# Optimization experiments

Hardware: AMD Instinct MI355X
Metric: run time of the kernel (lower is better)

Reference implementation:

```python
import jax, jax.numpy as jnp
import numpy as np

RATE = 0.1
RANDOM_PORTION = 0.1


def setup_inputs() -> dict:
    key = jax.random.key(0)
    x = jax.random.normal(key, (32, 524288), dtype=jnp.float32)
    return {"x": x}


def reference(x) -> jnp.ndarray:
    # Training-mode forward of RandomTopKModifier.
    b = x.shape[0]
    xf = x.reshape(b, -1)                      # [B, N]
    n = xf.shape[1]
    k = max(1, round(RATE * n))

    # 1) top-k by magnitude (indices only; unsorted is fine, set-equivalent)
    _, topk_idx = jax.lax.top_k(jnp.abs(xf), k)            # [B, k] int32

    # 2) build per-element sampling probabilities:
    #    random_portion mass spread over the N-k non-topk slots,
    #    (1 - random_portion) mass spread over the k topk slots.
    rows = jnp.arange(b)[:, None]                           # [B, 1]
    probs = jnp.full_like(xf, RANDOM_PORTION / (n - k))
    probs = probs.at[rows, topk_idx].set((1.0 - RANDOM_PORTION) / k)

    # 3) weighted sampling of k indices WITHOUT replacement
    #    (torch.multinomial(probs, k)) via the Gumbel-top-k trick.
    g = jax.random.gumbel(jax.random.key(42), xf.shape, dtype=xf.dtype)
    _, sel_idx = jax.lax.top_k(jnp.log(probs) + g, k)       # [B, k]

    # 4) scatter a binary mask and apply it
    mask = jnp.zeros_like(xf).at[rows, sel_idx].set(1.0)
    return (mask * xf).reshape(x.shape)
```

## Files before the change

kernel.cpp:

```cpp
#include <hip/hip_runtime.h>
#include <stdint.h>


static constexpr uint32_t BB = 32;
static constexpr uint32_t NN = 524288;
static constexpr uint32_t KK = 52429;
static constexpr uint32_t W = 64;
static constexpr uint32_t CHUNK = NN / W;
static constexpr uint32_t SEGCAP1 = 1024;
static constexpr uint32_t CAP1 = W * SEGCAP1;
static constexpr uint32_t SEGCAP2 = 1280;
static constexpr uint32_t CAP2 = W * SEGCAP2;
static constexpr uint32_t SELCAP = 512;
static constexpr uint32_t SENT = 0xFFFFFFFFu;
static constexpr uint32_t T1KEY = 0x3FD00000u;
static constexpr uint32_t LO1 = T1KEY;
static constexpr uint32_t LO2 = 0x3EC4CCCCu;

__device__ __forceinline__ float xla_logf(float xin) {
#pragma clang fp contract(off)
  float x = fmaxf(xin, __uint_as_float(0x00800000u));
  uint32_t bits = __float_as_uint(x);
  float e = (float)((int)(bits >> 23) - 126);
  x = __uint_as_float((bits & 0x807fffffu) | 0x3f000000u);
  bool mlt = x < 0.707106781186547524f;
  float tmp = mlt ? x : 0.0f;
  x = x - 1.0f;
  e = e - (mlt ? 1.0f : 0.0f);
  x = x + tmp;
  float x2 = x * x;
  float x3 = x2 * x;
  float y, y1, y2;
  y  = 7.0376836292E-2f * x + -1.1514610310E-1f;
  y1 = -1.2420140846E-1f * x + 1.4249322787E-1f;
  y2 = 2.0000714765E-1f * x + -2.4999993993E-1f;
  y  = y * x + 1.1676998740E-1f;
  y1 = y1 * x + -1.6668057665E-1f;
  y2 = y2 * x + 3.3333331174E-1f;
  y  = y * x3 + y1;
  y  = y * x3 + y2;
  y  = y * x3;
  y1 = e * -2.12194440e-4f;
  tmp = x2 * 0.5f;
  y = y + y1;
  x = x - tmp;
  y2 = e * 0.693359375f;
  x = x + y;
  x = x + y2;
  return x;
}

__device__ __forceinline__ float c_top_val()  { return xla_logf((float)((1.0 - 0.1) / 52429.0)); }
__device__ __forceinline__ float c_rand_val() { return xla_logf((float)(0.1 / 471859.0)); }

__device__ __forceinline__ uint32_t tf_bits(uint32_t i) {
  const uint32_t ks0 = 0u, ks1 = 42u, ks2 = 0x1BD11BDAu ^ 42u;
  uint32_t x0 = 0u + ks0;
  uint32_t x1 = i + ks1;
#define TFR(r) { x0 += x1; x1 = (x1 << (r)) | (x1 >> (32 - (r))); x1 ^= x0; }
  TFR(13) TFR(15) TFR(26) TFR(6)
  x0 += ks1; x1 += ks2 + 1u;
  TFR(17) TFR(29) TFR(16) TFR(24)
  x0 += ks2; x1 += ks0 + 2u;
  TFR(13) TFR(15) TFR(26) TFR(6)
  x0 += ks0; x1 += ks1 + 3u;
  TFR(17) TFR(29) TFR(16) TFR(24)
  x0 += ks1; x1 += ks2 + 4u;
  TFR(13) TFR(15) TFR(26) TFR(6)
  x0 += ks2; x1 += ks0 + 5u;
#undef TFR
  return x0 ^ x1;
}

__device__ __forceinline__ uint32_t key_x(float v) { return __float_as_uint(v) & 0x7fffffffu; }
__device__ __forceinline__ uint32_t key_s(float v) {
  uint32_t b = __float_as_uint(v);
  return (b & 0x80000000u) ? ~b : (b | 0x80000000u);
}


__global__ void __launch_bounds__(256)
k_candcoll1(const float* __restrict__ src,
            uint32_t* __restrict__ cidx, uint32_t* __restrict__ ckey) {
  __shared__ uint32_t lcnt;
  uint32_t row = blockIdx.y, seg = blockIdx.x;
  if (threadIdx.x == 0) lcnt = 0u;
  __syncthreads();
  uint32_t colbase = seg * CHUNK;
  uint32_t base = row * CAP1 + seg * SEGCAP1;
  const float4* p = (const float4*)(src + (size_t)row * NN + colbase);
  for (uint32_t j = threadIdx.x; j < CHUNK / 4; j += 256) {
    float4 v = p[j];
    float vv[4] = {v.x, v.y, v.z, v.w};
#pragma unroll
    for (int e = 0; e < 4; ++e) {
      uint32_t key = key_x(vv[e]);
      if (key >= T1KEY) {
        uint32_t li = atomicAdd(&lcnt, 1u);
        if (li < SEGCAP1) { cidx[base + li] = colbase + j * 4 + e; ckey[base + li] = key; }
      }
    }
  }
  __syncthreads();
  uint32_t c = (lcnt < SEGCAP1) ? lcnt : SEGCAP1;
  for (uint32_t j = c + threadIdx.x; j < SEGCAP1; j += 256) ckey[base + j] = SENT;
}

__device__ __forceinline__ void scan_hist(const uint32_t* lh, uint32_t* csA,
                                          uint32_t* sh, uint32_t kk, uint32_t t) {
  uint32_t s0 = 0;
  if (t < 256) {
#pragma unroll
    for (int j = 0; j < 8; ++j) s0 += lh[t * 8 + j];
    csA[t] = s0;
  }
  __syncthreads();
#pragma unroll
  for (uint32_t stp = 1; stp < 256; stp <<= 1) {
    uint32_t v = 0;
    if (t < 256 && t + stp < 256) v = csA[t + stp];
    __syncthreads();
    if (t < 256) csA[t] += v;
    __syncthreads();
  }
  if (t < 256) {
    uint32_t Sst = csA[t] - s0;
    if (Sst < kk && Sst + s0 >= kk) {
      uint32_t acc = Sst, bin = t * 8;
      for (int b2 = (int)t * 8 + 7; b2 >= (int)t * 8; --b2) {
        uint32_t hv = lh[b2];
        if (acc + hv >= kk) { bin = (uint32_t)b2; break; }
        acc += hv;
      }
      sh[0] = bin; sh[1] = kk - acc;
    }
  }
  __syncthreads();
}

__global__ void __launch_bounds__(1024)
k_select(const uint32_t* __restrict__ cidx, const uint32_t* __restrict__ ckey,
         uint32_t cap, uint32_t LO, uint32_t* __restrict__ st, uint32_t* __restrict__ sel) {
  __shared__ uint32_t lh[2048];
  __shared__ uint32_t csA[256];
  __shared__ uint32_t lkey[1024];
  __shared__ uint32_t lidx[1024];
  __shared__ uint32_t sh[8];
  uint32_t row = blockIdx.x;
  uint32_t t = threadIdx.x;
  const uint4* pk = (const uint4*)(ckey + (size_t)row * cap);
  for (uint32_t b = t; b < 2048; b += 1024) lh[b] = 0u;
  __syncthreads();
  for (uint32_t j0 = 0; j0 < cap / 4; j0 += 4 * 1024) {
    uint4 k4[4];
#pragma unroll
    for (int u = 0; u < 4; ++u) k4[u] = pk[j0 + u * 1024 + t];
#pragma unroll
    for (int u = 0; u < 4; ++u) {
      uint32_t kk[4] = {k4[u].x, k4[u].y, k4[u].z, k4[u].w};
#pragma unroll
      for (int e = 0; e < 4; ++e) {
        if (kk[e] != SENT) {
          uint32_t bin = (kk[e] - LO) >> 13;
          if (bin > 2047u) bin = 2047u;
          atomicAdd(&lh[bin], 1u);
        }
      }
    }
  }
  __syncthreads();
  scan_hist(lh, csA, sh, KK, t);
  uint32_t bstar = sh[0], kkW = sh[1];
  if (t == 0) sh[4] = 0u;
  __syncthreads();
  for (uint32_t j0 = 0; j0 < cap / 4; j0 += 4 * 1024) {
    uint4 k4[4];
#pragma unroll
    for (int u = 0; u < 4; ++u) k4[u] = pk[j0 + u * 1024 + t];
#pragma unroll
    for (int u = 0; u < 4; ++u) {
      uint32_t kk[4] = {k4[u].x, k4[u].y, k4[u].z, k4[u].w};
#pragma unroll
      for (int e = 0; e < 4; ++e) {
        if (kk[e] != SENT && ((kk[e] - LO) >> 13) == bstar) {
          uint32_t li = atomicAdd(&sh[4], 1u);
          if (li < 1024) { lkey[li] = kk[e]; lidx[li] = cidx[(size_t)row * cap + (j0 + u * 1024 + t) * 4 + e]; }
        }
      }
    }
  }
  __syncthreads();
  uint32_t cnt = sh[4]; if (cnt > 1024) cnt = 1024;
  if (t < cnt) {
    uint32_t myk = lkey[t], myi = lidx[t];
    uint32_t gt = 0, eq = 0, eqlt = 0;
    for (uint32_t b = 0; b < cnt; ++b) {
      uint32_t kb = lkey[b];
      gt += (kb > myk) ? 1u : 0u;
      if (kb == myk) { eq++; eqlt += (lidx[b] < myi) ? 1u : 0u; }
    }
    if (gt < kkW && gt + eq >= kkW) {
      uint32_t m = kkW - gt;
      if (eqlt == 0) { st[row * 8 + 2] = myk; st[row * 8 + 4] = (m > SELCAP) ? SELCAP : m; }
      if (eqlt < m && eqlt < SELCAP) sel[row * SELCAP + eqlt] = myi;
    }
  }
}

__global__ void __launch_bounds__(256)
k_compute_u(const float* __restrict__ x, const uint32_t* __restrict__ st1,
            const uint32_t* __restrict__ sel1,
            uint32_t* __restrict__ cidx, uint32_t* __restrict__ ckey) {
  __shared__ uint32_t lcnt;
  uint32_t row = blockIdx.y, seg = blockIdx.x;
  if (threadIdx.x == 0) lcnt = 0u;
  __syncthreads();
  const uint32_t BT = (uint32_t)ceilf(0.150f  * 8388608.0f) << 9;
  const uint32_t BR = (uint32_t)ceilf(0.9765f * 8388608.0f) << 9;
  uint32_t thr1 = st1[row * 8 + 2];
  uint32_t m1 = st1[row * 8 + 4];
  uint32_t colbase = seg * CHUNK;
  uint32_t base = row * CAP2 + seg * SEGCAP2;
  uint32_t ibase = (row << 19) + colbase;
  const float4* px = (const float4*)(x + (size_t)row * NN + colbase);
  for (uint32_t j = threadIdx.x; j < CHUNK / 4; j += 256) {
    float4 v = px[j];
    float vv[4] = {v.x, v.y, v.z, v.w};
#pragma unroll
    for (int e = 0; e < 4; ++e) {
      uint32_t col = colbase + j * 4 + e;
      uint32_t key = key_x(vv[e]);
      bool istop = key > thr1;
      if (key == thr1) {
        for (uint32_t q = 0; q < m1; ++q)
          if (sel1[row * SELCAP + q] == col) { istop = true; break; }
      }
      uint32_t b = tf_bits(ibase + j * 4 + e);
      if (b >= (istop ? BT : BR)) {
        uint32_t li = atomicAdd(&lcnt, 1u);
        if (li < SEGCAP2) {
          cidx[base + li] = col | (istop ? 0x80000000u : 0u);
          ckey[base + li] = b;
        }
      }
    }
  }
  __syncthreads();
  uint32_t c = (lcnt < SEGCAP2) ? lcnt : SEGCAP2;
  for (uint32_t j = c + threadIdx.x; j < SEGCAP2; j += 256) {
    cidx[base + j] = SENT;
    ckey[base + j] = SENT;
  }
}

__global__ void __launch_bounds__(256)
k_finish(uint32_t* __restrict__ cidx, uint32_t* __restrict__ ckey) {
  uint32_t row = blockIdx.y, seg = blockIdx.x;
  uint32_t base = row * CAP2 + seg * SEGCAP2;
  float CT = c_top_val(), CR = c_rand_val();
  for (uint32_t j = threadIdx.x; j < SEGCAP2; j += 256) {
    uint32_t ci = cidx[base + j];
    if (ci == SENT) continue;
    uint32_t b = ckey[base + j];
    float u = __uint_as_float((b >> 9) | 0x3f800000u) - 1.0f;
    u = fmaxf(u, 1.17549435e-38f);
    float nl = -xla_logf(u);
    float g = -xla_logf(nl);
    float s = ((ci >> 31) ? CT : CR) + g;
    ckey[base + j] = key_s(s);
    cidx[base + j] = ci & 0x7FFFFFFFu;
  }
}

__global__ void __launch_bounds__(256)
k_scatter(const float* __restrict__ x, float* __restrict__ out,
          const uint32_t* __restrict__ cidx, const uint32_t* __restrict__ ckey,
          const uint32_t* __restrict__ st2, const uint32_t* __restrict__ sel2) {
  uint32_t row = blockIdx.y, seg = blockIdx.x;
  uint32_t thr2 = st2[row * 8 + 2];
  uint32_t m2 = st2[row * 8 + 4];
  uint32_t base = row * CAP2 + seg * SEGCAP2;
  for (uint32_t j = threadIdx.x; j < SEGCAP2; j += 256) {
    uint32_t key = ckey[base + j];
    if (key == SENT) continue;
    uint32_t col = cidx[base + j];
    bool take = key > thr2;
    if (key == thr2) {
      for (uint32_t q = 0; q < m2; ++q)
        if (sel2[row * SELCAP + q] == col) { take = true; break; }
    }
    if (take) out[(size_t)row * NN + col] = x[(size_t)row * NN + col];
  }
}

extern "C" void kernel_launch(void* const* d_in, const int* in_sizes, int n_in,
                              void* d_out, int out_size, void* d_ws, size_t ws_size,
                              hipStream_t stream) {
  const float* x = (const float*)d_in[0];
  float* out = (float*)d_out;

  uint32_t* w = (uint32_t*)d_ws;
  uint32_t* st1   = w;
  uint32_t* st2   = st1 + BB * 8;
  uint32_t* sel1  = st2 + BB * 8;
  uint32_t* sel2  = sel1 + BB * SELCAP;
  uint32_t* cidx  = sel2 + BB * SELCAP;
  uint32_t* ckey  = cidx + BB * CAP2;

  dim3 blk(256), blkS(1024), gridF(W, BB), gridR(BB);

  k_candcoll1<<<gridF, blk, 0, stream>>>(x, cidx, ckey);
  k_select<<<gridR, blkS, 0, stream>>>(cidx, ckey, CAP1, LO1, st1, sel1);

  k_compute_u<<<gridF, blk, 0, stream>>>(x, st1, sel1, cidx, ckey);

  k_finish<<<gridF, blk, 0, stream>>>(cidx, ckey);

  k_select<<<gridR, blkS, 0, stream>>>(cidx, ckey, CAP2, LO2, st2, sel2);

  hipMemsetAsync(out, 0, (size_t)BB * NN * 4u, stream);
  k_scatter<<<gridF, blk, 0, stream>>>(x, out, cidx, ckey, st2, sel2);
}
```

Before: 149.8 us.

## Count high-magnitude elements and collect only a narrow window for top-k threshold

Measured after the change: 161.0 us. 7.4% more time.

```diff
diff --git a/kernel.cpp b/kernel.cpp
--- a/kernel.cpp
+++ b/kernel.cpp
@@ -7,13 +7,14 @@
 static constexpr uint32_t KK = 52429;
 static constexpr uint32_t W = 64;
 static constexpr uint32_t CHUNK = NN / W;
-static constexpr uint32_t SEGCAP1 = 1024;
-static constexpr uint32_t CAP1 = W * SEGCAP1;
+static constexpr uint32_t WINCAP1 = 256;
+static constexpr uint32_t WCAP1 = W * WINCAP1;
 static constexpr uint32_t SEGCAP2 = 1280;
 static constexpr uint32_t CAP2 = W * SEGCAP2;
 static constexpr uint32_t SELCAP = 512;
 static constexpr uint32_t SENT = 0xFFFFFFFFu;
 static constexpr uint32_t T1KEY = 0x3FD00000u;
+static constexpr uint32_t B1K   = 0x3FD47AE1u;
 static constexpr uint32_t LO1 = T1KEY;
 static constexpr uint32_t LO2 = 0x3EC4CCCCu;
 
@@ -80,30 +81,39 @@
 
 
 __global__ void __launch_bounds__(256)
-k_candcoll1(const float* __restrict__ src,
-            uint32_t* __restrict__ cidx, uint32_t* __restrict__ ckey) {
-  __shared__ uint32_t lcnt;
+k_candcoll1(const float* __restrict__ src, uint32_t* __restrict__ wcid,
+            uint32_t* __restrict__ wkey, uint32_t* __restrict__ count1) {
+  __shared__ uint32_t lwin, red[256];
   uint32_t row = blockIdx.y, seg = blockIdx.x;
-  if (threadIdx.x == 0) lcnt = 0u;
+  if (threadIdx.x == 0) lwin = 0u;
   __syncthreads();
   uint32_t colbase = seg * CHUNK;
-  uint32_t base = row * CAP1 + seg * SEGCAP1;
+  uint32_t wb = row * WCAP1 + seg * WINCAP1;
   const float4* p = (const float4*)(src + (size_t)row * NN + colbase);
+  uint32_t myhi = 0;
   for (uint32_t j = threadIdx.x; j < CHUNK / 4; j += 256) {
     float4 v = p[j];
     float vv[4] = {v.x, v.y, v.z, v.w};
 #pragma unroll
     for (int e = 0; e < 4; ++e) {
       uint32_t key = key_x(vv[e]);
-      if (key >= T1KEY) {
-        uint32_t li = atomicAdd(&lcnt, 1u);
-        if (li < SEGCAP1) { cidx[base + li] = colbase + j * 4 + e; ckey[base + li] = key; }
-      }
-    }
-  }
-  __syncthreads();
-  uint32_t c = (lcnt < SEGCAP1) ? lcnt : SEGCAP1;
-  for (uint32_t j = c + threadIdx.x; j < SEGCAP1; j += 256) ckey[base + j] = SENT;
+      myhi += (key >= B1K) ? 1u : 0u;
+      if (key >= T1KEY && key < B1K) {
+        uint32_t li = atomicAdd(&lwin, 1u);
+        if (li < WINCAP1) { wcid[wb + li] = colbase + j * 4 + e; wkey[wb + li] = key; }
+      }
+    }
+  }
+  __syncthreads();
+  red[threadIdx.x] = myhi;
+  __syncthreads();
+  for (uint32_t stp = 128; stp > 0; stp >>= 1) {
+    if (threadIdx.x < stp) red[threadIdx.x] += red[threadIdx.x + stp];
+    __syncthreads();
+  }
+  if (threadIdx.x == 0) atomicAdd(&count1[row], red[0]);
+  uint32_t cw = (lwin < WINCAP1) ? lwin : WINCAP1;
+  for (uint32_t j = cw + threadIdx.x; j < WINCAP1; j += 256) wkey[wb + j] = SENT;
 }
 
 __device__ __forceinline__ void scan_hist(const uint32_t* lh, uint32_t* csA,
@@ -140,7 +150,8 @@
 
 __global__ void __launch_bounds__(1024)
 k_select(const uint32_t* __restrict__ cidx, const uint32_t* __restrict__ ckey,
-         uint32_t cap, uint32_t LO, uint32_t* __restrict__ st, uint32_t* __restrict__ sel) {
+         uint32_t cap, uint32_t LO, const uint32_t* __restrict__ subp,
+         uint32_t* __restrict__ st, uint32_t* __restrict__ sel) {
   __shared__ uint32_t lh[2048];
   __shared__ uint32_t csA[256];
   __shared__ uint32_t lkey[1024];
@@ -148,6 +159,7 @@
   __shared__ uint32_t sh[8];
   uint32_t row = blockIdx.x;
   uint32_t t = threadIdx.x;
+  uint32_t kkT = KK - subp[row];
   const uint4* pk = (const uint4*)(ckey + (size_t)row * cap);
   for (uint32_t b = t; b < 2048; b += 1024) lh[b] = 0u;
   __syncthreads();
@@ -169,7 +181,7 @@
     }
   }
   __syncthreads();
-  scan_hist(lh, csA, sh, KK, t);
+  scan_hist(lh, csA, sh, kkT, t);
   uint32_t bstar = sh[0], kkW = sh[1];
   if (t == 0) sh[4] = 0u;
   __syncthreads();
@@ -300,24 +312,31 @@
   float* out = (float*)d_out;
 
   uint32_t* w = (uint32_t*)d_ws;
-  uint32_t* st1   = w;
-  uint32_t* st2   = st1 + BB * 8;
-  uint32_t* sel1  = st2 + BB * 8;
-  uint32_t* sel2  = sel1 + BB * SELCAP;
-  uint32_t* cidx  = sel2 + BB * SELCAP;
-  uint32_t* ckey  = cidx + BB * CAP2;
+  uint32_t* count1 = w;
+  uint32_t* zeros  = count1 + BB;
+  uint32_t* st1    = zeros + BB;
+  uint32_t* st2    = st1 + BB * 8;
+  uint32_t* sel1   = st2 + BB * 8;
+  uint32_t* sel2   = sel1 + BB * SELCAP;
+  uint32_t* wcid   = sel2 + BB * SELCAP;
+  uint32_t* wkey   = wcid + BB * WCAP1;
+  uint32_t* cidx2  = wkey + BB * WCAP1;
+  uint32_t* ckey2  = cidx2 + BB * CAP2;
 
   dim3 blk(256), blkS(1024), gridF(W, BB), gridR(BB);
 
-  k_candcoll1<<<gridF, blk, 0, stream>>>(x, cidx, ckey);
-  k_select<<<gridR, blkS, 0, stream>>>(cidx, ckey, CAP1, LO1, st1, sel1);
-
-  k_compute_u<<<gridF, blk, 0, stream>>>(x, st1, sel1, cidx, ckey);
-
-  k_finish<<<gridF, blk, 0, stream>>>(cidx, ckey);
-
-  k_select<<<gridR, blkS, 0, stream>>>(cidx, ckey, CAP2, LO2, st2, sel2);
+  hipMemsetAsync(count1, 0, 2 * BB * 4u, stream);
+
+  k_candcoll1<<<gridF, blk, 0, stream>>>(x, wcid, wkey, count1);
+
+  k_select<<<gridR, blkS, 0, stream>>>(wcid, wkey, WCAP1, LO1, count1, st1, sel1);
+
+  k_compute_u<<<gridF, blk, 0, stream>>>(x, st1, sel1, cidx2, ckey2);
+
+  k_finish<<<gridF, blk, 0, stream>>>(cidx2, ckey2);
+
+  k_select<<<gridR, blkS, 0, stream>>>(cidx2, ckey2, CAP2, LO2, zeros, st2, sel2);
 
   hipMemsetAsync(out, 0, (size_t)BB * NN * 4u, stream);
-  k_scatter<<<gridF, blk, 0, stream>>>(x, out, cidx, ckey, st2, sel2);
-}
+  k_scatter<<<gridF, blk, 0, stream>>>(x, out, cidx2, ckey2, st2, sel2);
+}
```
